# Kernel optimization log

Measured on AMD Instinct MI355X. Metric: run time of the kernel, lower is better.

## Reference

```python
import jax, jax.numpy as jnp
import numpy as np
import math

H = 4
D_MODEL = 512
OUT_DIM = D_MODEL // 2  # 256 (concat=True path)
D_K = OUT_DIM // H      # 64
N = 4096


def setup_inputs() -> dict:
    key0 = jax.random.key(0)
    ks = jax.random.split(key0, 12)
    s = 1.0 / math.sqrt(D_MODEL)
    inp = {
        "query": jax.random.normal(ks[0], (N, D_MODEL), dtype=jnp.float32),
        "key": jax.random.normal(ks[1], (N, D_MODEL), dtype=jnp.float32),
        "mask": jax.random.randint(ks[2], (N, N), 0, 2, dtype=jnp.int32),
        # 4 linears (q, k, q_v, k_v), each d_model -> out_dim
        "Wq": jax.random.normal(ks[3], (OUT_DIM, D_MODEL), dtype=jnp.float32) * s,
        "bq": jax.random.normal(ks[4], (OUT_DIM,), dtype=jnp.float32) * s,
        "Wk": jax.random.normal(ks[5], (OUT_DIM, D_MODEL), dtype=jnp.float32) * s,
        "bk": jax.random.normal(ks[6], (OUT_DIM,), dtype=jnp.float32) * s,
        "Wqv": jax.random.normal(ks[7], (OUT_DIM, D_MODEL), dtype=jnp.float32) * s,
        "bqv": jax.random.normal(ks[8], (OUT_DIM,), dtype=jnp.float32) * s,
        "Wkv": jax.random.normal(ks[9], (OUT_DIM, D_MODEL), dtype=jnp.float32) * s,
        "bkv": jax.random.normal(ks[10], (OUT_DIM,), dtype=jnp.float32) * s,
    }
    return inp


def _heads(x, W, b):
    # [N, d_model] @ W^T + b -> [N, out_dim] -> [h, N, d_k]
    y = x @ W.T + b
    return y.reshape(-1, H, D_K).transpose(1, 0, 2)


def reference(query, key, mask, Wq, bq, Wk, bk, Wqv, bqv, Wkv, bkv):
    q = _heads(query, Wq, bq)    # [h, Nq, d_k]
    k = _heads(key, Wk, bk)      # [h, Nk, d_k]
    qv = _heads(query, Wqv, bqv)  # [h, Nq, d_k]
    kv = _heads(key, Wkv, bkv)    # [h, Nk, d_k]

    scores = jnp.einsum("hqd,hkd->hqk", q, k) / math.sqrt(D_K)  # [h, Nq, Nk]
    scores = jnp.where(mask[None] == 0, jnp.float32(-1e9), scores)
    p = jax.nn.softmax(scores, axis=-1)  # attention weights per head

    # x1 = ELU(p @ k_v), x2 = ELU(p^T @ q_v); concat over heads.
    x1 = jax.nn.elu(jnp.einsum("hqk,hkd->hqd", p, kv))  # [h, Nq, d_k]
    x2 = jax.nn.elu(jnp.einsum("hqk,hqd->hkd", p, qv))  # [h, Nk, d_k]
    x1 = x1.transpose(1, 0, 2).reshape(-1, H * D_K)  # [Nq, out_dim]
    x2 = x2.transpose(1, 0, 2).reshape(-1, H * D_K)  # [Nk, out_dim]
    # Dropout omitted (inference / deterministic reference).
    return x1, x2, p
```

## Files before the change

kernel.cpp:

```cpp
#include <hip/hip_runtime.h>
#include <hip/hip_bf16.h>

#define NN 4096
#define DMODEL 512
#define ODIM 256
#define NHEAD 4
#define DKH 64
#define NKW 64

typedef __attribute__((ext_vector_type(8))) short short8;
typedef __attribute__((ext_vector_type(4))) short short4v;
typedef __attribute__((ext_vector_type(8))) __bf16 bf16x8;
typedef __attribute__((ext_vector_type(4))) float f32x4;

__device__ __forceinline__ short f2bf(float f) {
    unsigned u = __builtin_bit_cast(unsigned, f);
    u += 0x7fffu + ((u >> 16) & 1u);
    return (short)(u >> 16);
}
__device__ __forceinline__ float bf2f(short s) {
    unsigned u = ((unsigned)(unsigned short)s) << 16;
    return __builtin_bit_cast(float, u);
}
__device__ __forceinline__ f32x4 mfma16(short8 a, short8 b, f32x4 c) {
    return __builtin_amdgcn_mfma_f32_16x16x32_bf16(
        __builtin_bit_cast(bf16x8, a), __builtin_bit_cast(bf16x8, b), c, 0, 0, 0);
}

__global__ __launch_bounds__(256) void pack_mask_k(const int* __restrict__ mask,
                                                   unsigned long long* __restrict__ bits) {
    int tid = blockIdx.x * 256 + threadIdx.x;
    int wid = tid >> 6;
    int lane = tid & 63;
    int v = mask[(size_t)wid * 64 + lane];
    unsigned long long b = __ballot(v != 0);
    if (lane == 0) bits[wid] = b;
}

__global__ __launch_bounds__(256) void proj_k(
    const float* __restrict__ Xq, const float* __restrict__ Xk,
    const float* __restrict__ Wq, const float* __restrict__ bq,
    const float* __restrict__ Wk, const float* __restrict__ bk,
    const float* __restrict__ Wqv, const float* __restrict__ bqv,
    const float* __restrict__ Wkv, const float* __restrict__ bkv,
    short* __restrict__ qh, short* __restrict__ kh,
    short* __restrict__ qvT, short* __restrict__ kvT) {
    int z = blockIdx.z;
    const float *X, *W, *B;
    short* out;
    int tr;
    float postscale = 1.f;
    switch (z) {
        case 0: X = Xq; W = Wq;  B = bq;  out = qh;  tr = 0; postscale = 0.125f; break;
        case 1: X = Xk; W = Wk;  B = bk;  out = kh;  tr = 0; break;
        case 2: X = Xq; W = Wqv; B = bqv; out = qvT; tr = 1; break;
        default: X = Xk; W = Wkv; B = bkv; out = kvT; tr = 1; break;
    }
    int lane = threadIdx.x & 63, w = threadIdx.x >> 6;
    int lr = lane & 15, lg = lane >> 4;
    int m0 = blockIdx.x * 64 + (w >> 1) * 32;
    int n0 = blockIdx.y * 64 + (w & 1) * 32;

    f32x4 acc[2][2] = {};
    for (int kk = 0; kk < DMODEL; kk += 32) {
        short8 a[2], b[2];
#pragma unroll
        for (int i = 0; i < 2; i++) {
            const float* pa = X + (size_t)(m0 + i * 16 + lr) * DMODEL + kk + lg * 8;
            const float* pb = W + (size_t)(n0 + i * 16 + lr) * DMODEL + kk + lg * 8;
            float4 a0 = *(const float4*)pa;
            float4 a1 = *(const float4*)(pa + 4);
            float4 b0 = *(const float4*)pb;
            float4 b1 = *(const float4*)(pb + 4);
            a[i][0] = f2bf(a0.x); a[i][1] = f2bf(a0.y); a[i][2] = f2bf(a0.z); a[i][3] = f2bf(a0.w);
            a[i][4] = f2bf(a1.x); a[i][5] = f2bf(a1.y); a[i][6] = f2bf(a1.z); a[i][7] = f2bf(a1.w);
            b[i][0] = f2bf(b0.x); b[i][1] = f2bf(b0.y); b[i][2] = f2bf(b0.z); b[i][3] = f2bf(b0.w);
            b[i][4] = f2bf(b1.x); b[i][5] = f2bf(b1.y); b[i][6] = f2bf(b1.z); b[i][7] = f2bf(b1.w);
        }
#pragma unroll
        for (int i = 0; i < 2; i++)
#pragma unroll
            for (int j = 0; j < 2; j++) acc[i][j] = mfma16(a[i], b[j], acc[i][j]);
    }
#pragma unroll
    for (int i = 0; i < 2; i++)
#pragma unroll
        for (int j = 0; j < 2; j++) {
            int col = n0 + j * 16 + lr;
            float bv = B[col];
            int hh = col >> 6, dk = col & 63;
#pragma unroll
            for (int r = 0; r < 4; r++) {
                int row = m0 + i * 16 + lg * 4 + r;
                short s = f2bf((acc[i][j][r] + bv) * postscale);
                if (!tr) out[((size_t)hh * NN + row) * DKH + dk] = s;
                else     out[((size_t)hh * DKH + dk) * NN + row] = s;
            }
        }
}

__global__ __launch_bounds__(512) void attn_fused_k(
    const short* __restrict__ qh, const short* __restrict__ kh, const short* __restrict__ kvT,
    const unsigned long long* __restrict__ bits,
    short* __restrict__ pbuf, float* __restrict__ linv_ws,
    float* __restrict__ x1_out, float* __restrict__ p_out) {
    int h = blockIdx.y;
    int strip = blockIdx.x;
    int tid = threadIdx.x, lane = tid & 63, w = tid >> 6;
    int lr = lane & 15, lg = lane >> 4;
    int q0 = strip * 16;

    __shared__ float smemf[4608];
    short (*plds)[16][72] = (short (*)[16][72])smemf;
    float (*xbuf)[64][17] = (float (*)[64][17])smemf;
    __shared__ float sl[8][16];
    __shared__ float linv_s[16];

    const short* khh = kh + (size_t)h * NN * DKH;
    const unsigned long long* brow = bits + (size_t)(q0 + lr) * NKW;
    short* ptile0 = pbuf + (((size_t)(h * 256 + strip) * 64) << 10);

    short8 bq[2];
#pragma unroll
    for (int kk = 0; kk < 2; kk++)
        bq[kk] = *(const short8*)(qh + ((size_t)h * NN + q0 + lr) * DKH + kk * 32 + lg * 8);

    float lrun = 0.f;
    f32x4 acc1[4] = {};
    for (int t = 0; t < 8; t++) {
        int kt = w * 8 + t;
        f32x4 s[4] = {};
#pragma unroll
        for (int fj = 0; fj < 4; fj++)
#pragma unroll
            for (int kk = 0; kk < 2; kk++) {
                short8 a = *(const short8*)(khh + (size_t)(kt * 64 + fj * 16 + lr) * DKH + kk * 32 + lg * 8);
                s[fj] = mfma16(a, bq[kk], s[fj]);
            }
        unsigned long long mw = brow[kt] >> (lg * 4);
        short* ptile = ptile0 + ((size_t)kt << 10);
#pragma unroll
        for (int fj = 0; fj < 4; fj++) {
            short4v pb4;
#pragma unroll
            for (int r = 0; r < 4; r++) {
                bool keep = (mw >> (fj * 16 + r)) & 1ull;
                float e = __expf(keep ? s[fj][r] : -100.f);
                lrun += e;
                pb4[r] = f2bf(e);
            }
            *(short4v*)&plds[w][lr][fj * 16 + lg * 4] = pb4;
            *(short4v*)(ptile + lr * 64 + fj * 16 + lg * 4) = pb4;
        }
#pragma unroll
        for (int kk = 0; kk < 2; kk++) {
            short8 a1 = *(const short8*)&plds[w][lr][kk * 32 + lg * 8];
#pragma unroll
            for (int fd = 0; fd < 4; fd++) {
                short8 bv = *(const short8*)(kvT + ((size_t)h * DKH + fd * 16 + lr) * NN + kt * 64 + kk * 32 + lg * 8);
                acc1[fd] = mfma16(a1, bv, acc1[fd]);
            }
        }
    }
    lrun += __shfl_xor(lrun, 16);
    lrun += __shfl_xor(lrun, 32);
    if (lg == 0) sl[w][lr] = lrun;
    __syncthreads();
    float l = 0.f;
#pragma unroll
    for (int w2 = 0; w2 < 8; w2++) l += sl[w2][lr];
    float linv = l > 0.f ? 1.f / l : 0.f;
    if (w == 0 && lg == 0) {
        linv_s[lr] = linv;
        linv_ws[(size_t)h * NN + q0 + lr] = linv;
    }
    __syncthreads();

    asm volatile("s_waitcnt vmcnt(0)" ::: "memory");
    const short* psrc0 = ptile0 + (size_t)(w * 8 + (lane >> 3)) * 1024 + (lane & 7) * 8;
    float* pdst0 = p_out + ((size_t)h * NN + q0) * NN + w * 512 + lane * 8;
#pragma unroll 4
    for (int r = 0; r < 16; r++) {
        short8 pv = *(const short8*)(psrc0 + r * 64);
        float lim = linv_s[r];
        float4 o0, o1;
        o0.x = bf2f(pv[0]) * lim; o0.y = bf2f(pv[1]) * lim;
        o0.z = bf2f(pv[2]) * lim; o0.w = bf2f(pv[3]) * lim;
        o1.x = bf2f(pv[4]) * lim; o1.y = bf2f(pv[5]) * lim;
        o1.z = bf2f(pv[6]) * lim; o1.w = bf2f(pv[7]) * lim;
        float* dst = pdst0 + (size_t)r * NN;
        *(float4*)dst = o0;
        *(float4*)(dst + 4) = o1;
    }

    __syncthreads();
    if (w >= 4) {
#pragma unroll
        for (int fd = 0; fd < 4; fd++)
#pragma unroll
            for (int r = 0; r < 4; r++) xbuf[w - 4][lane][fd * 4 + r] = acc1[fd][r];
    }
    __syncthreads();
    if (w < 4) {
#pragma unroll
        for (int fd = 0; fd < 4; fd++)
#pragma unroll
            for (int r = 0; r < 4; r++) acc1[fd][r] += xbuf[w][lane][fd * 4 + r];
    }
    __syncthreads();
    if (w >= 1 && w < 4) {
#pragma unroll
        for (int fd = 0; fd < 4; fd++)
#pragma unroll
            for (int r = 0; r < 4; r++) xbuf[w - 1][lane][fd * 4 + r] = acc1[fd][r];
    }
    __syncthreads();
    if (w == 0) {
#pragma unroll
        for (int fd = 0; fd < 4; fd++)
#pragma unroll
            for (int r = 0; r < 4; r++) {
                float v = acc1[fd][r] + xbuf[0][lane][fd * 4 + r] + xbuf[1][lane][fd * 4 + r] +
                          xbuf[2][lane][fd * 4 + r];
                v *= linv_s[lg * 4 + r];
                v = v > 0.f ? v : (__expf(v) - 1.f);
                x1_out[(size_t)(q0 + lg * 4 + r) * ODIM + h * DKH + fd * 16 + lr] = v;
            }
    }
}

__global__ __launch_bounds__(256) void scale_qv_k(const short* __restrict__ qvT,
                                                  const float* __restrict__ linv,
                                                  short* __restrict__ qvS) {
    int idx = blockIdx.x * 256 + threadIdx.x;
    int q8 = idx & 511;
    int dh = idx >> 9;
    int h = dh >> 6;
    short8 v = *(const short8*)(qvT + (size_t)dh * NN + q8 * 8);
    const float* lp = linv + (size_t)h * NN + q8 * 8;
    float4 l0 = *(const float4*)lp;
    float4 l1 = *(const float4*)(lp + 4);
    short8 o;
    o[0] = f2bf(bf2f(v[0]) * l0.x); o[1] = f2bf(bf2f(v[1]) * l0.y);
    o[2] = f2bf(bf2f(v[2]) * l0.z); o[3] = f2bf(bf2f(v[3]) * l0.w);
    o[4] = f2bf(bf2f(v[4]) * l1.x); o[5] = f2bf(bf2f(v[5]) * l1.y);
    o[6] = f2bf(bf2f(v[6]) * l1.z); o[7] = f2bf(bf2f(v[7]) * l1.w);
    *(short8*)(qvS + (size_t)dh * NN + q8 * 8) = o;
}

__global__ __launch_bounds__(512) void px2b_k(
    const short* __restrict__ pbuf, const short* __restrict__ qvS,
    float* __restrict__ x2part) {
    int kt = blockIdx.x, h = blockIdx.y, z = blockIdx.z;
    int tid = threadIdx.x, lane = tid & 63, w = tid >> 6;
    int fj = w & 3, sh = w >> 2;
    int lr = lane & 15, lg = lane >> 4;

    __shared__ float red[4][64][17];

    const short* qvh = qvS + (size_t)h * DKH * NN;
    f32x4 acc[4] = {};
    int qbase = z * 2048 + sh * 1024;
    for (int it = 0; it < 32; it++) {
        int qq = qbase + it * 32;
        int strip = (qq >> 4) + (lg >> 1);
        const short* ab = pbuf + (((size_t)(h * 256 + strip) * 64 + kt) << 10) +
                          (lg & 1) * 512 + fj * 16 + lr;
        short8 af;
#pragma unroll
        for (int j = 0; j < 8; j++) af[j] = ab[j * 64];
#pragma unroll
        for (int fd = 0; fd < 4; fd++) {
            short8 bv = *(const short8*)(qvh + (size_t)(fd * 16 + lr) * NN + qq + lg * 8);
            acc[fd] = mfma16(af, bv, acc[fd]);
        }
    }
    if (sh == 1) {
#pragma unroll
        for (int fd = 0; fd < 4; fd++)
#pragma unroll
            for (int r = 0; r < 4; r++) red[fj][lane][fd * 4 + r] = acc[fd][r];
    }
    __syncthreads();
    if (sh == 0) {
        float* xp = x2part + (size_t)z * NN * ODIM;
#pragma unroll
        for (int fd = 0; fd < 4; fd++)
#pragma unroll
            for (int r = 0; r < 4; r++) {
                float v = acc[fd][r] + red[fj][lane][fd * 4 + r];
                xp[(size_t)(kt * 64 + fj * 16 + lg * 4 + r) * ODIM + h * DKH + fd * 16 + lr] = v;
            }
    }
}

__global__ __launch_bounds__(256) void combine_x2_k(const float* __restrict__ x2part,
                                                    float* __restrict__ x2_out) {
    int idx = blockIdx.x * 256 + threadIdx.x;
    size_t i = (size_t)idx * 4;
    float4 a = *(const float4*)(x2part + i);
    float4 b = *(const float4*)(x2part + (size_t)NN * ODIM + i);
    float4 o;
    o.x = a.x + b.x; o.y = a.y + b.y; o.z = a.z + b.z; o.w = a.w + b.w;
    o.x = o.x > 0.f ? o.x : (__expf(o.x) - 1.f);
    o.y = o.y > 0.f ? o.y : (__expf(o.y) - 1.f);
    o.z = o.z > 0.f ? o.z : (__expf(o.z) - 1.f);
    o.w = o.w > 0.f ? o.w : (__expf(o.w) - 1.f);
    *(float4*)(x2_out + i) = o;
}

__global__ __launch_bounds__(512) void attn_fb_k(
    const short* __restrict__ qh, const short* __restrict__ kh, const short* __restrict__ kvT,
    const unsigned long long* __restrict__ bits,
    float* __restrict__ x1_out, float* __restrict__ p_out) {
    int h = blockIdx.y;
    int tid = threadIdx.x, lane = tid & 63, w = tid >> 6;
    int lr = lane & 15, lg = lane >> 4;
    int q0 = blockIdx.x * 16;

    __shared__ float smemf[4608];
    short (*plds)[16][72] = (short (*)[16][72])smemf;
    float (*xbuf)[64][17] = (float (*)[64][17])smemf;
    __shared__ float sl[8][16];

    const short* khh = kh + (size_t)h * NN * DKH;
    const unsigned long long* brow = bits + (size_t)(q0 + lr) * NKW;

    short8 bq[2];
#pragma unroll
    for (int kk = 0; kk < 2; kk++)
        bq[kk] = *(const short8*)(qh + ((size_t)h * NN + q0 + lr) * DKH + kk * 32 + lg * 8);

    float lrun = 0.f;
    for (int t = 0; t < 8; t++) {
        int kt = w * 8 + t;
        f32x4 s[4] = {};
#pragma unroll
        for (int fj = 0; fj < 4; fj++)
#pragma unroll
            for (int kk = 0; kk < 2; kk++) {
                short8 a = *(const short8*)(khh + (size_t)(kt * 64 + fj * 16 + lr) * DKH + kk * 32 + lg * 8);
                s[fj] = mfma16(a, bq[kk], s[fj]);
            }
        unsigned long long mw = brow[kt] >> (lg * 4);
#pragma unroll
        for (int fj = 0; fj < 4; fj++)
#pragma unroll
            for (int r = 0; r < 4; r++) {
                bool keep = (mw >> (fj * 16 + r)) & 1ull;
                lrun += __expf(keep ? s[fj][r] : -100.f);
            }
    }
    lrun += __shfl_xor(lrun, 16);
    lrun += __shfl_xor(lrun, 32);
    if (lg == 0) sl[w][lr] = lrun;
    __syncthreads();
    float l = 0.f;
#pragma unroll
    for (int w2 = 0; w2 < 8; w2++) l += sl[w2][lr];
    float linv = l > 0.f ? 1.f / l : 0.f;

    f32x4 acc1[4] = {};
    float* prow = p_out + ((size_t)h * NN + q0 + lr) * NN;
    for (int t = 0; t < 8; t++) {
        int kt = w * 8 + t;
        f32x4 s[4] = {};
#pragma unroll
        for (int fj = 0; fj < 4; fj++)
#pragma unroll
            for (int kk = 0; kk < 2; kk++) {
                short8 a = *(const short8*)(khh + (size_t)(kt * 64 + fj * 16 + lr) * DKH + kk * 32 + lg * 8);
                s[fj] = mfma16(a, bq[kk], s[fj]);
            }
        unsigned long long mw = brow[kt] >> (lg * 4);
#pragma unroll
        for (int fj = 0; fj < 4; fj++) {
            float4 pv;
            short4v pb;
#pragma unroll
            for (int r = 0; r < 4; r++) {
                bool keep = (mw >> (fj * 16 + r)) & 1ull;
                float p = __expf(keep ? s[fj][r] : -100.f) * linv;
                (&pv.x)[r] = p;
                pb[r] = f2bf(p);
            }
            *(float4*)(prow + kt * 64 + fj * 16 + lg * 4) = pv;
            *(short4v*)&plds[w][lr][fj * 16 + lg * 4] = pb;
        }
#pragma unroll
        for (int kk = 0; kk < 2; kk++) {
            short8 a1 = *(const short8*)&plds[w][lr][kk * 32 + lg * 8];
#pragma unroll
            for (int fd = 0; fd < 4; fd++) {
                short8 bv = *(const short8*)(kvT + ((size_t)h * DKH + fd * 16 + lr) * NN + kt * 64 + kk * 32 + lg * 8);
                acc1[fd] = mfma16(a1, bv, acc1[fd]);
            }
        }
    }
    __syncthreads();
    if (w >= 4) {
#pragma unroll
        for (int fd = 0; fd < 4; fd++)
#pragma unroll
            for (int r = 0; r < 4; r++) xbuf[w - 4][lane][fd * 4 + r] = acc1[fd][r];
    }
    __syncthreads();
    if (w < 4) {
#pragma unroll
        for (int fd = 0; fd < 4; fd++)
#pragma unroll
            for (int r = 0; r < 4; r++) acc1[fd][r] += xbuf[w][lane][fd * 4 + r];
    }
    __syncthreads();
    if (w >= 1 && w < 4) {
#pragma unroll
        for (int fd = 0; fd < 4; fd++)
#pragma unroll
            for (int r = 0; r < 4; r++) xbuf[w - 1][lane][fd * 4 + r] = acc1[fd][r];
    }
    __syncthreads();
    if (w == 0) {
#pragma unroll
        for (int fd = 0; fd < 4; fd++)
#pragma unroll
            for (int r = 0; r < 4; r++) {
                float v = acc1[fd][r] + xbuf[0][lane][fd * 4 + r] + xbuf[1][lane][fd * 4 + r] +
                          xbuf[2][lane][fd * 4 + r];
                v = v > 0.f ? v : (__expf(v) - 1.f);
                x1_out[(size_t)(q0 + lg * 4 + r) * ODIM + h * DKH + fd * 16 + lr] = v;
            }
    }
}

__global__ __launch_bounds__(512) void px2_fb_k(
    const float* __restrict__ p, const short* __restrict__ qvT,
    float* __restrict__ x2_out) {
    int h = blockIdx.y;
    int k0 = blockIdx.x * 32;
    int tid = threadIdx.x, lane = tid & 63, w = tid >> 6;
    int lr = lane & 15, lg = lane >> 4;

    __shared__ float red[4][64][33];

    f32x4 acc[2][4] = {};
    const float* pbase = p + (size_t)h * NN * NN;
    const short* qvh = qvT + (size_t)h * DKH * NN;

    for (int it = 0; it < 16; it++) {
        int qq = w * 512 + it * 32;
        short8 aP[2];
#pragma unroll
        for (int fj = 0; fj < 2; fj++) {
            const float* pp = pbase + (size_t)(qq + lg * 8) * NN + k0 + fj * 16 + lr;
            short8 av;
#pragma unroll
            for (int j = 0; j < 8; j++) av[j] = f2bf(pp[j * NN]);
            aP[fj] = av;
        }
#pragma unroll
        for (int fd = 0; fd < 4; fd++) {
            short8 bv = *(const short8*)(qvh + (size_t)(fd * 16 + lr) * NN + qq + lg * 8);
#pragma unroll
            for (int fj = 0; fj < 2; fj++) acc[fj][fd] = mfma16(aP[fj], bv, acc[fj][fd]);
        }
    }
    if (w >= 4) {
#pragma unroll
        for (int fj = 0; fj < 2; fj++)
#pragma unroll
            for (int fd = 0; fd < 4; fd++)
#pragma unroll
                for (int r = 0; r < 4; r++)
                    red[w - 4][lane][fj * 16 + fd * 4 + r] = acc[fj][fd][r];
    }
    __syncthreads();
    if (w < 4) {
#pragma unroll
        for (int fj = 0; fj < 2; fj++)
#pragma unroll
            for (int fd = 0; fd < 4; fd++)
#pragma unroll
                for (int r = 0; r < 4; r++)
                    acc[fj][fd][r] += red[w][lane][fj * 16 + fd * 4 + r];
    }
    __syncthreads();
    if (w >= 1 && w < 4) {
#pragma unroll
        for (int fj = 0; fj < 2; fj++)
#pragma unroll
            for (int fd = 0; fd < 4; fd++)
#pragma unroll
                for (int r = 0; r < 4; r++)
                    red[w - 1][lane][fj * 16 + fd * 4 + r] = acc[fj][fd][r];
    }
    __syncthreads();
    if (w == 0) {
#pragma unroll
        for (int fj = 0; fj < 2; fj++)
#pragma unroll
            for (int fd = 0; fd < 4; fd++)
#pragma unroll
                for (int r = 0; r < 4; r++) {
                    float v = acc[fj][fd][r];
#pragma unroll
                    for (int s2 = 0; s2 < 3; s2++) v += red[s2][lane][fj * 16 + fd * 4 + r];
                    v = v > 0.f ? v : (__expf(v) - 1.f);
                    x2_out[(size_t)(k0 + fj * 16 + lg * 4 + r) * ODIM + h * DKH + fd * 16 + lr] = v;
                }
    }
}

extern "C" void kernel_launch(void* const* d_in, const int* in_sizes, int n_in,
                              void* d_out, int out_size, void* d_ws, size_t ws_size,
                              hipStream_t stream) {
    (void)in_sizes; (void)n_in; (void)out_size;
    const float* query = (const float*)d_in[0];
    const float* key   = (const float*)d_in[1];
    const int*   mask  = (const int*)d_in[2];
    const float* Wq  = (const float*)d_in[3];
    const float* bq  = (const float*)d_in[4];
    const float* Wk  = (const float*)d_in[5];
    const float* bk  = (const float*)d_in[6];
    const float* Wqv = (const float*)d_in[7];
    const float* bqv = (const float*)d_in[8];
    const float* Wkv = (const float*)d_in[9];
    const float* bkv = (const float*)d_in[10];

    float* out = (float*)d_out;
    float* x1 = out;
    float* x2 = out + (size_t)NN * ODIM;
    float* p  = out + (size_t)2 * NN * ODIM;

    char* ws = (char*)d_ws;
    short* qh  = (short*)(ws);
    short* kh  = (short*)(ws + (2ull << 20));
    short* qvT = (short*)(ws + (4ull << 20));
    short* kvT = (short*)(ws + (6ull << 20));
    unsigned long long* bits = (unsigned long long*)(ws + (8ull << 20));
    float* linv_ws = (float*)(ws + (10ull << 20));
    short* qvS = (short*)(ws + (10ull << 20) + (1ull << 19));
    float* x2part = (float*)(ws + (13ull << 20));
    short* pbuf = (short*)(ws + (21ull << 20));
    size_t need = (21ull << 20) + (size_t)NHEAD * NN * NN * sizeof(short);

    hipLaunchKernelGGL(pack_mask_k, dim3(NN * NN / 64 / 4), dim3(256), 0, stream, mask, bits);
    hipLaunchKernelGGL(proj_k, dim3(64, 4, 4), dim3(256), 0, stream,
                       query, key, Wq, bq, Wk, bk, Wqv, bqv, Wkv, bkv, qh, kh, qvT, kvT);

    if (ws_size >= need) {
        hipLaunchKernelGGL(attn_fused_k, dim3(NN / 16, NHEAD), dim3(512), 0, stream,
                           qh, kh, kvT, bits, pbuf, linv_ws, x1, p);
        hipLaunchKernelGGL(scale_qv_k, dim3(512), dim3(256), 0, stream, qvT, linv_ws, qvS);
        hipLaunchKernelGGL(px2b_k, dim3(NN / 64, NHEAD, 2), dim3(512), 0, stream,
                           pbuf, qvS, x2part);
        hipLaunchKernelGGL(combine_x2_k, dim3(NN * ODIM / 4 / 256), dim3(256), 0, stream,
                           x2part, x2);
    } else {
        hipLaunchKernelGGL(attn_fb_k, dim3(NN / 16, NHEAD), dim3(512), 0, stream,
                           qh, kh, kvT, bits, x1, p);
        hipLaunchKernelGGL(px2_fb_k, dim3(NN / 32, NHEAD), dim3(512), 0, stream,
                           p, qvT, x2);
    }
}
```

Measured before the change: 369.3 us.

## Stage P tiles through LDS in px2b and use nontemporal mask loads/P stores

The px2b kernel previously gathered the transposed A fragment straight from global memory with strided scalar short loads. It now cooperatively copies 16 P tiles per round into padded shared memory with vectorized 16-byte loads, then gathers the fragments from LDS. The intent is to replace uncoalesced global loads with coalesced ones, at the cost of extra LDS use and barriers per round. Separately, the mask read in pack_mask_k and the large fp32 P output write now use nontemporal load/store to reduce cache pollution from streaming data.

```diff
diff --git a/kernel.cpp b/kernel.cpp
--- a/kernel.cpp
+++ b/kernel.cpp
@@ -32,7 +32,7 @@
     int tid = blockIdx.x * 256 + threadIdx.x;
     int wid = tid >> 6;
     int lane = tid & 63;
-    int v = mask[(size_t)wid * 64 + lane];
+    int v = __builtin_nontemporal_load(mask + (size_t)wid * 64 + lane);
     unsigned long long b = __ballot(v != 0);
     if (lane == 0) bits[wid] = b;
 }
@@ -183,14 +183,14 @@
     for (int r = 0; r < 16; r++) {
         short8 pv = *(const short8*)(psrc0 + r * 64);
         float lim = linv_s[r];
-        float4 o0, o1;
-        o0.x = bf2f(pv[0]) * lim; o0.y = bf2f(pv[1]) * lim;
-        o0.z = bf2f(pv[2]) * lim; o0.w = bf2f(pv[3]) * lim;
-        o1.x = bf2f(pv[4]) * lim; o1.y = bf2f(pv[5]) * lim;
-        o1.z = bf2f(pv[6]) * lim; o1.w = bf2f(pv[7]) * lim;
+        f32x4 o0, o1;
+        o0[0] = bf2f(pv[0]) * lim; o0[1] = bf2f(pv[1]) * lim;
+        o0[2] = bf2f(pv[2]) * lim; o0[3] = bf2f(pv[3]) * lim;
+        o1[0] = bf2f(pv[4]) * lim; o1[1] = bf2f(pv[5]) * lim;
+        o1[2] = bf2f(pv[6]) * lim; o1[3] = bf2f(pv[7]) * lim;
         float* dst = pdst0 + (size_t)r * NN;
-        *(float4*)dst = o0;
-        *(float4*)(dst + 4) = o1;
+        __builtin_nontemporal_store(o0, (f32x4*)dst);
+        __builtin_nontemporal_store(o1, (f32x4*)(dst + 4));
     }
 
     __syncthreads();
@@ -256,23 +256,45 @@
     int fj = w & 3, sh = w >> 2;
     int lr = lane & 15, lg = lane >> 4;
 
+    __shared__ short stg[16 * 1040];
     __shared__ float red[4][64][17];
 
     const short* qvh = qvS + (size_t)h * DKH * NN;
     f32x4 acc[4] = {};
-    int qbase = z * 2048 + sh * 1024;
-    for (int it = 0; it < 32; it++) {
-        int qq = qbase + it * 32;
-        int strip = (qq >> 4) + (lg >> 1);
-        const short* ab = pbuf + (((size_t)(h * 256 + strip) * 64 + kt) << 10) +
-                          (lg & 1) * 512 + fj * 16 + lr;
-        short8 af;
-#pragma unroll
-        for (int j = 0; j < 8; j++) af[j] = ab[j * 64];
-#pragma unroll
-        for (int fd = 0; fd < 4; fd++) {
-            short8 bv = *(const short8*)(qvh + (size_t)(fd * 16 + lr) * NN + qq + lg * 8);
-            acc[fd] = mfma16(af, bv, acc[fd]);
+
+    int stile = tid >> 5;
+    int inner = tid & 31;
+
+    for (int r = 0; r < 8; r++) {
+        int s0 = z * 128 + r * 16;
+        __syncthreads();
+        {
+            const short* src = pbuf + (((size_t)(h * 256 + s0 + stile) * 64 + kt) << 10) + inner * 32;
+            short* dst = stg + stile * 1040 + inner * 32;
+            short8 v0 = *(const short8*)(src);
+            short8 v1 = *(const short8*)(src + 8);
+            short8 v2 = *(const short8*)(src + 16);
+            short8 v3 = *(const short8*)(src + 24);
+            *(short8*)(dst) = v0;
+            *(short8*)(dst + 8) = v1;
+            *(short8*)(dst + 16) = v2;
+            *(short8*)(dst + 24) = v3;
+        }
+        __syncthreads();
+        int rq = z * 2048 + r * 256;
+#pragma unroll
+        for (int p2 = 0; p2 < 4; p2++) {
+            int pr = sh * 4 + p2;
+            int qq = rq + pr * 32;
+            const short* tb = stg + (pr * 2 + (lg >> 1)) * 1040 + ((lg & 1) * 8) * 64 + fj * 16 + lr;
+            short8 af;
+#pragma unroll
+            for (int j = 0; j < 8; j++) af[j] = tb[j * 64];
+#pragma unroll
+            for (int fd = 0; fd < 4; fd++) {
+                short8 bv = *(const short8*)(qvh + (size_t)(fd * 16 + lr) * NN + qq + lg * 8);
+                acc[fd] = mfma16(af, bv, acc[fd]);
+            }
         }
     }
     if (sh == 1) {
```

After: 379.8 us. +2.8%, slower.

## Transpose bf16 P tile layout, split x2 reduction four ways, nontemporal mask loads

Applied to the files above, without the earlier changes.

Stores each 16x64 bf16 probability tile key-major (transposed), so the P^T@qv kernel can fetch its MFMA A-fragment with a single 16-byte load instead of eight strided 2-byte loads. The fp32 P writeback is reworked to read the transposed tiles and emit scalar stores coalesced across lanes. The x2 kernel's query range is split into four z-partitions to double block count, with the combine kernel summing four partials and the workspace grown to fit them. Mask loads are made nontemporal. The trade-off is scalar P stores and scattered 2-byte LDS-free global writes of the tile, plus extra partial-buffer traffic.

```diff
diff --git a/kernel.cpp b/kernel.cpp
--- a/kernel.cpp
+++ b/kernel.cpp
@@ -32,7 +32,7 @@
     int tid = blockIdx.x * 256 + threadIdx.x;
     int wid = tid >> 6;
     int lane = tid & 63;
-    int v = mask[(size_t)wid * 64 + lane];
+    int v = __builtin_nontemporal_load(mask + (size_t)wid * 64 + lane);
     unsigned long long b = __ballot(v != 0);
     if (lane == 0) bits[wid] = b;
 }
@@ -150,7 +150,9 @@
                 pb4[r] = f2bf(e);
             }
             *(short4v*)&plds[w][lr][fj * 16 + lg * 4] = pb4;
-            *(short4v*)(ptile + lr * 64 + fj * 16 + lg * 4) = pb4;
+#pragma unroll
+            for (int r = 0; r < 4; r++)
+                ptile[(fj * 16 + lg * 4 + r) * 16 + lr] = pb4[r];
         }
 #pragma unroll
         for (int kk = 0; kk < 2; kk++) {
@@ -177,20 +179,22 @@
     __syncthreads();
 
     asm volatile("s_waitcnt vmcnt(0)" ::: "memory");
-    const short* psrc0 = ptile0 + (size_t)(w * 8 + (lane >> 3)) * 1024 + (lane & 7) * 8;
-    float* pdst0 = p_out + ((size_t)h * NN + q0) * NN + w * 512 + lane * 8;
-#pragma unroll 4
-    for (int r = 0; r < 16; r++) {
-        short8 pv = *(const short8*)(psrc0 + r * 64);
-        float lim = linv_s[r];
-        float4 o0, o1;
-        o0.x = bf2f(pv[0]) * lim; o0.y = bf2f(pv[1]) * lim;
-        o0.z = bf2f(pv[2]) * lim; o0.w = bf2f(pv[3]) * lim;
-        o1.x = bf2f(pv[4]) * lim; o1.y = bf2f(pv[5]) * lim;
-        o1.z = bf2f(pv[6]) * lim; o1.w = bf2f(pv[7]) * lim;
-        float* dst = pdst0 + (size_t)r * NN;
-        *(float4*)dst = o0;
-        *(float4*)(dst + 4) = o1;
+    float linvv[16];
+#pragma unroll
+    for (int j = 0; j < 16; j++) linvv[j] = linv_s[j];
+    for (int t = 0; t < 8; t++) {
+        int kt = w * 8 + t;
+        const short* tl = ptile0 + ((size_t)kt << 10) + lane * 16;
+        float* pd = p_out + ((size_t)h * NN + q0) * NN + kt * 64 + lane;
+#pragma unroll
+        for (int qh2 = 0; qh2 < 2; qh2++) {
+            short8 pv = *(const short8*)(tl + qh2 * 8);
+#pragma unroll
+            for (int j = 0; j < 8; j++) {
+                int q = qh2 * 8 + j;
+                pd[(size_t)q * NN] = bf2f(pv[j]) * linvv[q];
+            }
+        }
     }
 
     __syncthreads();
@@ -260,15 +264,15 @@
 
     const short* qvh = qvS + (size_t)h * DKH * NN;
     f32x4 acc[4] = {};
-    int qbase = z * 2048 + sh * 1024;
-    for (int it = 0; it < 32; it++) {
+    int qbase = z * 1024 + sh * 512;
+
+#pragma unroll 4
+    for (int it = 0; it < 16; it++) {
         int qq = qbase + it * 32;
         int strip = (qq >> 4) + (lg >> 1);
-        const short* ab = pbuf + (((size_t)(h * 256 + strip) * 64 + kt) << 10) +
-                          (lg & 1) * 512 + fj * 16 + lr;
-        short8 af;
-#pragma unroll
-        for (int j = 0; j < 8; j++) af[j] = ab[j * 64];
+        const short* ap = pbuf + (((size_t)(h * 256 + strip) * 64 + kt) << 10) +
+                          (fj * 16 + lr) * 16 + (lg & 1) * 8;
+        short8 af = *(const short8*)ap;
 #pragma unroll
         for (int fd = 0; fd < 4; fd++) {
             short8 bv = *(const short8*)(qvh + (size_t)(fd * 16 + lr) * NN + qq + lg * 8);
@@ -298,10 +302,16 @@
                                                     float* __restrict__ x2_out) {
     int idx = blockIdx.x * 256 + threadIdx.x;
     size_t i = (size_t)idx * 4;
+    const size_t stride = (size_t)NN * ODIM;
     float4 a = *(const float4*)(x2part + i);
-    float4 b = *(const float4*)(x2part + (size_t)NN * ODIM + i);
+    float4 b = *(const float4*)(x2part + stride + i);
+    float4 c = *(const float4*)(x2part + 2 * stride + i);
+    float4 d = *(const float4*)(x2part + 3 * stride + i);
     float4 o;
-    o.x = a.x + b.x; o.y = a.y + b.y; o.z = a.z + b.z; o.w = a.w + b.w;
+    o.x = a.x + b.x + c.x + d.x;
+    o.y = a.y + b.y + c.y + d.y;
+    o.z = a.z + b.z + c.z + d.z;
+    o.w = a.w + b.w + c.w + d.w;
     o.x = o.x > 0.f ? o.x : (__expf(o.x) - 1.f);
     o.y = o.y > 0.f ? o.y : (__expf(o.y) - 1.f);
     o.z = o.z > 0.f ? o.z : (__expf(o.z) - 1.f);
@@ -540,8 +550,8 @@
     float* linv_ws = (float*)(ws + (10ull << 20));
     short* qvS = (short*)(ws + (10ull << 20) + (1ull << 19));
     float* x2part = (float*)(ws + (13ull << 20));
-    short* pbuf = (short*)(ws + (21ull << 20));
-    size_t need = (21ull << 20) + (size_t)NHEAD * NN * NN * sizeof(short);
+    short* pbuf = (short*)(ws + (29ull << 20));
+    size_t need = (29ull << 20) + (size_t)NHEAD * NN * NN * sizeof(short);
 
     hipLaunchKernelGGL(pack_mask_k, dim3(NN * NN / 64 / 4), dim3(256), 0, stream, mask, bits);
     hipLaunchKernelGGL(proj_k, dim3(64, 4, 4), dim3(256), 0, stream,
@@ -551,7 +561,7 @@
         hipLaunchKernelGGL(attn_fused_k, dim3(NN / 16, NHEAD), dim3(512), 0, stream,
                            qh, kh, kvT, bits, pbuf, linv_ws, x1, p);
         hipLaunchKernelGGL(scale_qv_k, dim3(512), dim3(256), 0, stream, qvT, linv_ws, qvS);
-        hipLaunchKernelGGL(px2b_k, dim3(NN / 64, NHEAD, 2), dim3(512), 0, stream,
+        hipLaunchKernelGGL(px2b_k, dim3(NN / 64, NHEAD, 4), dim3(512), 0, stream,
                            pbuf, qvS, x2part);
         hipLaunchKernelGGL(combine_x2_k, dim3(NN * ODIM / 4 / 256), dim3(256), 0, stream,
                            x2part, x2);
```

Measured after the change: 359.8 us. 1.03x faster.
